# Kernel optimization log

Measured on AMD Instinct MI355X. Metric: run time of the kernel, lower is better.

## Reference

```python
import jax, jax.numpy as jnp
import numpy as np


def setup_inputs() -> dict:
    key = jax.random.key(0)
    ks = jax.random.split(key, 11)
    B, S, D, K = 8, 2048, 512, 256
    s = lambda k, shp, fan: jax.random.normal(k, shp, dtype=jnp.float32) / np.sqrt(fan)
    return {
        "x": jax.random.normal(ks[0], (B, S, D), dtype=jnp.float32),
        "Wk1": s(ks[1], (D, K), D), "bk1": jnp.zeros((K,), jnp.float32),
        "Wq1": s(ks[2], (D, K), D), "bq1": jnp.zeros((K,), jnp.float32),
        "Wk2": s(ks[3], (D, K), D), "bk2": jnp.zeros((K,), jnp.float32),
        "Wq2": s(ks[4], (D, K), D), "bq2": jnp.zeros((K,), jnp.float32),
        "Wv2": s(ks[5], (D, D), D), "bv2": jnp.zeros((D,), jnp.float32),
    }


def _attn(q, k, v):
    # raw scores with NO 1/sqrt(d) scaling, softmax over key axis, then AV
    scores = jax.nn.softmax(jnp.einsum('bqd,bkd->bqk', q, k), axis=-1)
    return jnp.einsum('bqk,bkd->bqd', scores, v)


def _block2(h, Wk2, bk2, Wq2, bq2, Wv2, bv2):
    k = h @ Wk2 + bk2
    q = h @ Wq2 + bq2
    v = h @ Wv2 + bv2
    v = v / jnp.linalg.norm(v, axis=2, keepdims=True)  # L2-normalize values
    return _attn(q, k, v)


def reference(x, Wk1, bk1, Wq1, bq1, Wk2, bk2, Wq2, bq2, Wv2, bv2):
    # block 1: values are the raw input x
    k1 = x @ Wk1 + bk1
    q1 = x @ Wq1 + bq1
    outputs = _attn(q1, k1, x)
    # blocks 2 and 3 reuse the SAME layer-2 weights (as in the torch forward)
    hidden = _block2(outputs, Wk2, bk2, Wq2, bq2, Wv2, bv2)
    final = _block2(hidden, Wk2, bk2, Wq2, bq2, Wv2, bv2)
    return final[0, -1, :]
```

## Files before the change

kernel.cpp:

```cpp
#include <hip/hip_runtime.h>
#include <math.h>

typedef __attribute__((ext_vector_type(8))) short short8;
typedef __attribute__((ext_vector_type(4))) float f32x4;
typedef unsigned short ushort_t;

__device__ inline unsigned short f2bf_rn(float f) {
    unsigned u = __builtin_bit_cast(unsigned, f);
    u += 0x7FFF + ((u >> 16) & 1);
    return (unsigned short)(u >> 16);
}
__device__ inline float bf2f(unsigned short h) {
    unsigned u = ((unsigned)h) << 16;
    return __builtin_bit_cast(float, u);
}

#define ISSUE(ST, RA, RB)                                                      \
  do {                                                                         \
    int s_ = (ST);                                                             \
    int sg_ = s_ / SPS;                                                        \
    int k0_ = (s_ - sg_ * SPS) * 64;                                           \
    const unsigned short* Ap_ = (sg_ < 2) ? Ah : Al;                           \
    const unsigned short* Bp_ = (sg_ == 1) ? Bl : Bh;                          \
    _Pragma("unroll") for (int i_ = 0; i_ < 4; ++i_) {                         \
      RA[i_] = *(const uint4*)(Ap_ + (size_t)(bm + crow[i_]) * lda + k0_ + csl[i_] * 8); \
      RB[i_] = *(const uint4*)(Bp_ + (size_t)(bn + crow[i_]) * ldb + k0_ + csl[i_] * 8); \
    }                                                                          \
  } while (0)

#define PHASE(IT, RWa, RWb, RLa, RLb)                                          \
  do {                                                                         \
    _Pragma("unroll") for (int i_ = 0; i_ < 4; ++i_) {                         \
      int wsl_ = csl[i_] ^ (crow[i_] & 7);                                     \
      *(uint4*)&As[crow[i_]][wsl_ * 8] = RWa[i_];                              \
      *(uint4*)&Bs[crow[i_]][wsl_ * 8] = RWb[i_];                              \
    }                                                                          \
    if ((IT) + 1 < CHUNK) { ISSUE(st0 + (IT) + 1, RLa, RLb); }                 \
    asm volatile("s_waitcnt lgkmcnt(0)\n\ts_barrier" ::: "memory");            \
    _Pragma("unroll") for (int kk = 0; kk < 2; ++kk) {                         \
      short8 af[4], bf[4];                                                     \
      _Pragma("unroll") for (int f = 0; f < 4; ++f) {                          \
        int ar = wm * 64 + f * 16 + r15;                                       \
        int as_ = (kk * 4 + ksl) ^ (ar & 7);                                   \
        af[f] = *(const short8*)&As[ar][as_ * 8];                              \
        int br = wn * 64 + f * 16 + r15;                                       \
        int bs_ = (kk * 4 + ksl) ^ (br & 7);                                   \
        bf[f] = *(const short8*)&Bs[br][bs_ * 8];                              \
      }                                                                        \
      _Pragma("unroll") for (int i_ = 0; i_ < 4; ++i_)                         \
        _Pragma("unroll") for (int j_ = 0; j_ < 4; ++j_)                       \
          acc[i_][j_] = __builtin_amdgcn_mfma_f32_16x16x32_bf16(               \
              af[i_], bf[j_], acc[i_][j_], 0, 0, 0);                           \
    }                                                                          \
    asm volatile("s_barrier" ::: "memory");                                    \
  } while (0)

template <int KSEG, int NSPLIT>
__global__ __launch_bounds__(256, 2) void gemm_bf16(
    const unsigned short* __restrict__ Ah, const unsigned short* __restrict__ Al, int lda,
    const unsigned short* __restrict__ Bh, const unsigned short* __restrict__ Bl, int ldb,
    float* __restrict__ Cout, int ldc)
{
    constexpr int SPS = KSEG / 64;
    constexpr int NST = 3 * SPS;
    constexpr int CHUNK = NST / NSPLIT;

    __shared__ __align__(16) unsigned short As[128][64];
    __shared__ __align__(16) unsigned short Bs[128][64];

    const int tid = threadIdx.x, lane = tid & 63, w = tid >> 6;
    const int wm = w >> 1, wn = w & 1;
    const int bm = blockIdx.y * 128, bn = blockIdx.x * 128;
    const int st0 = blockIdx.z * CHUNK;
    const int r15 = lane & 15, ksl = lane >> 4;

    int crow[4], csl[4];
#pragma unroll
    for (int i = 0; i < 4; ++i) { int c = tid + i * 256; crow[i] = c >> 3; csl[i] = c & 7; }

    f32x4 acc[4][4];
#pragma unroll
    for (int i = 0; i < 4; ++i)
#pragma unroll
        for (int j = 0; j < 4; ++j) acc[i][j] = (f32x4){0.f, 0.f, 0.f, 0.f};

    uint4 rA0[4], rB0[4], rA1[4], rB1[4];
    ISSUE(st0, rA0, rB0);

#pragma unroll 1
    for (int it = 0; it < CHUNK; it += 2) {
        PHASE(it,     rA0, rB0, rA1, rB1);
        PHASE(it + 1, rA1, rB1, rA0, rB0);
    }

    float* Cz = Cout + (size_t)blockIdx.z * (size_t)(gridDim.y * 128) * ldc;
#pragma unroll
    for (int i = 0; i < 4; ++i) {
        int rowb = bm + wm * 64 + i * 16 + (lane >> 4) * 4;
#pragma unroll
        for (int j = 0; j < 4; ++j) {
            int colb = bn + wn * 64 + j * 16 + r15;
#pragma unroll
            for (int r = 0; r < 4; ++r)
                Cz[(size_t)(rowb + r) * ldc + colb] = acc[i][j][r];
        }
    }
}

template <int NS, bool BIAS>
__global__ __launch_bounds__(256) void reduce_kernel(
    const float* __restrict__ part, size_t pstride4,
    const float* __restrict__ bias, float* __restrict__ C,
    unsigned short* __restrict__ Ch, unsigned short* __restrict__ Cl, int N)
{
    size_t idx = (size_t)blockIdx.x * 256 + threadIdx.x;
    const float4* p = (const float4*)part;
    float4 s = p[idx];
#pragma unroll
    for (int z = 1; z < NS; ++z) {
        float4 t = p[idx + (size_t)z * pstride4];
        s.x += t.x; s.y += t.y; s.z += t.z; s.w += t.w;
    }
    if (BIAS) {
        int col = (int)((idx * 4) & (size_t)(N - 1));
        s.x += bias[col]; s.y += bias[col + 1]; s.z += bias[col + 2]; s.w += bias[col + 3];
    }
    ((float4*)C)[idx] = s;
    float v[4] = {s.x, s.y, s.z, s.w};
    unsigned short h[4], l[4];
#pragma unroll
    for (int q = 0; q < 4; ++q) { h[q] = f2bf_rn(v[q]); l[q] = f2bf_rn(v[q] - bf2f(h[q])); }
    uint2 hp = make_uint2((unsigned)h[0] | ((unsigned)h[1] << 16), (unsigned)h[2] | ((unsigned)h[3] << 16));
    uint2 lp = make_uint2((unsigned)l[0] | ((unsigned)l[1] << 16), (unsigned)l[2] | ((unsigned)l[3] << 16));
    ((uint2*)Ch)[idx] = hp;
    ((uint2*)Cl)[idx] = lp;
}

#define SLK(r, s) ((s) ^ (((s) >> 3) & 3) ^ ((((r) ^ ((r) >> 3))) & 7))

__global__ __launch_bounds__(256, 2) void flash_attn(
    const unsigned short* __restrict__ Qh, const unsigned short* __restrict__ Ql,
    const unsigned short* __restrict__ Kh, const unsigned short* __restrict__ Kl,
    int ldqk,
    const unsigned short* __restrict__ VTh, const unsigned short* __restrict__ VTl,
    float* __restrict__ Opart, float* __restrict__ Mpart, float* __restrict__ Lpart)
{
    const int tid = threadIdx.x, lane = tid & 63, w = tid >> 6;
    const int z = blockIdx.x;
    const int q0 = blockIdx.y * 64;
    const int s0 = z * 256;
    const int cc = lane & 15, g = lane >> 4;

    __shared__ __align__(16) unsigned short KsH[32][256], KsL[32][256];
    __shared__ __align__(16) unsigned short PsH[64][32], PsL[64][32];
    __shared__ float Fs[64];
    __shared__ int flagAny[4];

    short8 qh[8], qlv[8];
#pragma unroll
    for (int ks = 0; ks < 8; ++ks) {
        const size_t qoff = (size_t)(q0 + w * 16 + cc) * ldqk + ks * 32 + g * 8;
        qh[ks]  = *(const short8*)(Qh + qoff);
        qlv[ks] = *(const short8*)(Ql + qoff);
    }

    f32x4 acc[4][8];
#pragma unroll
    for (int a = 0; a < 4; ++a)
#pragma unroll
        for (int b = 0; b < 8; ++b) acc[a][b] = (f32x4){0.f, 0.f, 0.f, 0.f};
    float m[4] = {-1e30f, -1e30f, -1e30f, -1e30f};
    float l[4] = {0.f, 0.f, 0.f, 0.f};

#pragma unroll 1
    for (int sub = 0; sub < 8; ++sub) {
        __syncthreads();
#pragma unroll
        for (int i = 0; i < 4; ++i) {
            int idx = tid + i * 256;
            int row = (idx >> 3) & 31;
            int sl  = (idx & 7) | ((idx >> 8) << 3);
            size_t go = (size_t)(s0 + sub * 32 + row) * ldqk + sl * 8;
            uint4 vh = *(const uint4*)(Kh + go);
            uint4 vl = *(const uint4*)(Kl + go);
            int sw = SLK(row, sl);
            *(uint4*)&KsH[row][sw * 8] = vh;
            *(uint4*)&KsL[row][sw * 8] = vl;
        }
        __syncthreads();

        f32x4 sac[2];
        sac[0] = (f32x4){0.f, 0.f, 0.f, 0.f};
        sac[1] = (f32x4){0.f, 0.f, 0.f, 0.f};
#pragma unroll
        for (int ks = 0; ks < 8; ++ks) {
#pragma unroll
            for (int t = 0; t < 2; ++t) {
                int row = t * 16 + cc;
                int sw = SLK(row, ks * 4 + g);
                short8 bh = *(const short8*)&KsH[row][sw * 8];
                short8 bl = *(const short8*)&KsL[row][sw * 8];
                sac[t] = __builtin_amdgcn_mfma_f32_16x16x32_bf16(qh[ks], bh, sac[t], 0, 0, 0);
                sac[t] = __builtin_amdgcn_mfma_f32_16x16x32_bf16(qh[ks], bl, sac[t], 0, 0, 0);
                sac[t] = __builtin_amdgcn_mfma_f32_16x16x32_bf16(qlv[ks], bh, sac[t], 0, 0, 0);
            }
        }

        float mt[4], fr[4];
        bool nb = false;
#pragma unroll
        for (int r = 0; r < 4; ++r) {
            float v = fmaxf(sac[0][r], sac[1][r]);
#pragma unroll
            for (int o = 8; o >= 1; o >>= 1) v = fmaxf(v, __shfl_xor(v, o));
            mt[r] = v;
            nb = nb || (v > m[r] + 8.f);
        }
        const int need = __any((int)nb);
        if (need) {
#pragma unroll
            for (int r = 0; r < 4; ++r) {
                float mn = fmaxf(m[r], mt[r]);
                fr[r] = __expf(m[r] - mn);
                m[r] = mn;
                l[r] *= fr[r];
            }
        } else {
#pragma unroll
            for (int r = 0; r < 4; ++r) fr[r] = 1.f;
        }
        if (cc == 0) {
#pragma unroll
            for (int r = 0; r < 4; ++r) Fs[w * 16 + g * 4 + r] = fr[r];
        }
        if (lane == 0) flagAny[w] = need;

#pragma unroll
        for (int t = 0; t < 2; ++t) {
            float ps[4];
#pragma unroll
            for (int r = 0; r < 4; ++r) {
                float p = __expf(sac[t][r] - m[r]);
                ps[r] = p;
                unsigned short ph = f2bf_rn(p);
                unsigned short pl = f2bf_rn(p - bf2f(ph));
                int qq = w * 16 + g * 4 + r;
                int kv = cc + 16 * t;
                int col = (((kv >> 3) ^ (qq & 3)) << 3) | (kv & 7);
                PsH[qq][col] = ph;
                PsL[qq][col] = pl;
            }
#pragma unroll
            for (int r = 0; r < 4; ++r) {
                float s = ps[r];
#pragma unroll
                for (int o = 8; o >= 1; o >>= 1) s += __shfl_xor(s, o);
                l[r] += s;
            }
        }
        __syncthreads();

        int anyf = flagAny[0] | flagAny[1] | flagAny[2] | flagAny[3];
        if (anyf) {
#pragma unroll
            for (int qt = 0; qt < 4; ++qt)
#pragma unroll
                for (int r = 0; r < 4; ++r) {
                    float fq = Fs[qt * 16 + g * 4 + r];
#pragma unroll
                    for (int dt = 0; dt < 8; ++dt) acc[qt][dt][r] *= fq;
                }
        }

        short8 pah[4], pal[4];
#pragma unroll
        for (int qt = 0; qt < 4; ++qt) {
            int qr = qt * 16 + cc;
            int col = (g ^ (qr & 3)) << 3;
            pah[qt] = *(const short8*)&PsH[qr][col];
            pal[qt] = *(const short8*)&PsL[qr][col];
        }
#pragma unroll
        for (int dt = 0; dt < 8; ++dt) {
            size_t vo = (size_t)(w * 128 + dt * 16 + cc) * 2048 + s0 + sub * 32 + g * 8;
            short8 vh = *(const short8*)(VTh + vo);
            short8 vl = *(const short8*)(VTl + vo);
#pragma unroll
            for (int qt = 0; qt < 4; ++qt) {
                acc[qt][dt] = __builtin_amdgcn_mfma_f32_16x16x32_bf16(pah[qt], vh, acc[qt][dt], 0, 0, 0);
                acc[qt][dt] = __builtin_amdgcn_mfma_f32_16x16x32_bf16(pah[qt], vl, acc[qt][dt], 0, 0, 0);
                acc[qt][dt] = __builtin_amdgcn_mfma_f32_16x16x32_bf16(pal[qt], vh, acc[qt][dt], 0, 0, 0);
            }
        }
    }

#pragma unroll
    for (int qt = 0; qt < 4; ++qt)
#pragma unroll
        for (int dt = 0; dt < 8; ++dt)
#pragma unroll
            for (int r = 0; r < 4; ++r) {
                int row = q0 + qt * 16 + g * 4 + r;
                int col = w * 128 + dt * 16 + cc;
                Opart[((size_t)z * 2048 + row) * 512 + col] = acc[qt][dt][r];
            }
    if (cc == 0) {
#pragma unroll
        for (int r = 0; r < 4; ++r) {
            int row = q0 + w * 16 + g * 4 + r;
            Mpart[z * 2048 + row] = m[r];
            Lpart[z * 2048 + row] = l[r];
        }
    }
}

__global__ __launch_bounds__(256) void flash_combine(
    const float* __restrict__ Opart, const float* __restrict__ Mpart,
    const float* __restrict__ Lpart,
    unsigned short* __restrict__ Oh, unsigned short* __restrict__ Ol)
{
    const int q = blockIdx.x;
    const int tid = threadIdx.x;
    float wz[8];
    float mstar = -1e30f;
#pragma unroll
    for (int zz = 0; zz < 8; ++zz) { wz[zz] = Mpart[zz * 2048 + q]; mstar = fmaxf(mstar, wz[zz]); }
    float L = 0.f;
#pragma unroll
    for (int zz = 0; zz < 8; ++zz) {
        float e = __expf(wz[zz] - mstar);
        L += e * Lpart[zz * 2048 + q];
        wz[zz] = e;
    }
    float invL = 1.f / L;
    int d = tid * 2;
    float sx = 0.f, sy = 0.f;
#pragma unroll
    for (int zz = 0; zz < 8; ++zz) {
        const float2 t = *(const float2*)(Opart + ((size_t)zz * 2048 + q) * 512 + d);
        sx += wz[zz] * t.x;
        sy += wz[zz] * t.y;
    }
    sx *= invL; sy *= invL;
    unsigned short h0 = f2bf_rn(sx), h1 = f2bf_rn(sy);
    unsigned short l0 = f2bf_rn(sx - bf2f(h0)), l1 = f2bf_rn(sy - bf2f(h1));
    *(unsigned*)(Oh + (size_t)q * 512 + d) = (unsigned)h0 | ((unsigned)h1 << 16);
    *(unsigned*)(Ol + (size_t)q * 512 + d) = (unsigned)l0 | ((unsigned)l1 << 16);
}

__global__ __launch_bounds__(256) void l2norm_kernel(float* __restrict__ V, int ld,
                                                     int coloff, int D)
{
    __shared__ float red[8];
    const int tid = threadIdx.x;
    float* p = V + (size_t)blockIdx.x * ld + coloff;
    float s = 0.f;
    for (int i = tid; i < D; i += 256) { float v = p[i]; s = fmaf(v, v, s); }
#pragma unroll
    for (int o = 32; o; o >>= 1) s += __shfl_down(s, o);
    if ((tid & 63) == 0) red[tid >> 6] = s;
    __syncthreads();
    float scale = 1.f / sqrtf(red[0] + red[1] + red[2] + red[3]);
    for (int i = tid; i < D; i += 256) p[i] *= scale;
}

__global__ __launch_bounds__(256) void tc_kernel(
    const float* __restrict__ in, int ldin,
    unsigned short* __restrict__ oh, unsigned short* __restrict__ ol,
    int ldo, int rowoff)
{
    __shared__ float tile[32][33];
    int bx = blockIdx.x * 32, by = blockIdx.y * 32;
    int tx = threadIdx.x & 31, ty = threadIdx.x >> 5;
#pragma unroll
    for (int i = 0; i < 32; i += 8)
        tile[ty + i][tx] = in[(size_t)(by + ty + i) * ldin + bx + tx];
    __syncthreads();
#pragma unroll
    for (int i = 0; i < 32; i += 8) {
        float v = tile[tx][ty + i];
        unsigned short h = f2bf_rn(v);
        unsigned short l = f2bf_rn(v - bf2f(h));
        size_t o = (size_t)(rowoff + bx + ty + i) * ldo + by + tx;
        oh[o] = h; ol[o] = l;
    }
}

__global__ __launch_bounds__(256) void convert_hl(
    const float* __restrict__ in, unsigned short* __restrict__ oh,
    unsigned short* __restrict__ ol)
{
    size_t idx = (size_t)blockIdx.x * 256 + threadIdx.x;
    float4 s = ((const float4*)in)[idx];
    float v[4] = {s.x, s.y, s.z, s.w};
    unsigned short h[4], l[4];
#pragma unroll
    for (int q = 0; q < 4; ++q) { h[q] = f2bf_rn(v[q]); l[q] = f2bf_rn(v[q] - bf2f(h[q])); }
    uint2 hp = make_uint2((unsigned)h[0] | ((unsigned)h[1] << 16), (unsigned)h[2] | ((unsigned)h[3] << 16));
    uint2 lp = make_uint2((unsigned)l[0] | ((unsigned)l[1] << 16), (unsigned)l[2] | ((unsigned)l[3] << 16));
    ((uint2*)oh)[idx] = hp;
    ((uint2*)ol)[idx] = lp;
}

__global__ __launch_bounds__(256) void concat_bias(
    const float* bk1, const float* bq1, const float* bk2, const float* bq2,
    const float* bv2, float* b1, float* b2)
{
    int i = blockIdx.x * 256 + threadIdx.x;
    if (i < 512) b1[i] = (i < 256) ? bk1[i] : bq1[i - 256];
    if (i < 1024) b2[i] = (i < 256) ? bk2[i] : (i < 512 ? bq2[i - 256] : bv2[i - 512]);
}

template <bool HAS_BIAS>
__global__ __launch_bounds__(256) void gemv_nt(
    const float* __restrict__ a, const float* __restrict__ Bt, int ldb,
    const float* __restrict__ bias, float* __restrict__ out, int K)
{
    int w = threadIdx.x >> 6, lane = threadIdx.x & 63;
    int n = blockIdx.x * 4 + w;
    const float* row = Bt + (size_t)n * ldb;
    float s = 0.f;
    for (int k = lane; k < K; k += 64) s = fmaf(a[k], row[k], s);
#pragma unroll
    for (int o = 32; o; o >>= 1) s += __shfl_down(s, o);
    if (lane == 0) out[n] = HAS_BIAS ? s + bias[n] : s;
}

__global__ __launch_bounds__(256) void gemv_hl(
    const float* __restrict__ p, const unsigned short* __restrict__ Vh,
    const unsigned short* __restrict__ Vl, int ld, float* __restrict__ out, int K)
{
    int w = threadIdx.x >> 6, lane = threadIdx.x & 63;
    int d = blockIdx.x * 4 + w;
    const unsigned short* rh = Vh + (size_t)d * ld;
    const unsigned short* rl = Vl + (size_t)d * ld;
    float s = 0.f;
    for (int k = lane; k < K; k += 64) s = fmaf(p[k], bf2f(rh[k]) + bf2f(rl[k]), s);
#pragma unroll
    for (int o = 32; o; o >>= 1) s += __shfl_down(s, o);
    if (lane == 0) out[d] = s;
}

__global__ __launch_bounds__(256) void softmax_f32(float* __restrict__ S, int L)
{
    __shared__ float row[2048];
    __shared__ float red[8];
    const int tid = threadIdx.x;
    float* p = S + (size_t)blockIdx.x * L;
    float mx = -1e30f;
    for (int i = tid; i < L; i += 256) { float v = p[i]; row[i] = v; mx = fmaxf(mx, v); }
#pragma unroll
    for (int o = 32; o; o >>= 1) mx = fmaxf(mx, __shfl_down(mx, o));
    if ((tid & 63) == 0) red[tid >> 6] = mx;
    __syncthreads();
    mx = fmaxf(fmaxf(red[0], red[1]), fmaxf(red[2], red[3]));
    float sum = 0.f;
    for (int i = tid; i < L; i += 256) { float e = expf(row[i] - mx); row[i] = e; sum += e; }
#pragma unroll
    for (int o = 32; o; o >>= 1) sum += __shfl_down(sum, o);
    __syncthreads();
    if ((tid & 63) == 0) red[4 + (tid >> 6)] = sum;
    __syncthreads();
    float inv = 1.f / (red[4] + red[5] + red[6] + red[7]);
    for (int i = tid; i < L; i += 256) p[i] = row[i] * inv;
}

extern "C" void kernel_launch(void* const* d_in, const int* in_sizes, int n_in,
                              void* d_out, int out_size, void* d_ws, size_t ws_size,
                              hipStream_t stream)
{
    const float* x   = (const float*)d_in[0];
    const float* Wk1 = (const float*)d_in[1];
    const float* bk1 = (const float*)d_in[2];
    const float* Wq1 = (const float*)d_in[3];
    const float* bq1 = (const float*)d_in[4];
    const float* Wk2 = (const float*)d_in[5];
    const float* bk2 = (const float*)d_in[6];
    const float* Wq2 = (const float*)d_in[7];
    const float* bq2 = (const float*)d_in[8];
    const float* Wv2 = (const float*)d_in[9];
    const float* bv2 = (const float*)d_in[10];
    float* out = (float*)d_out;

    const int S = 2048, D = 512;
    typedef unsigned short us;

    char* p = (char*)d_ws;
    float* C   = (float*)p;  p += (size_t)S * 1024 * 4;
    float* BIG = (float*)p;  p += (size_t)8 * S * 512 * 4;
    float* Mp  = (float*)p;  p += (size_t)8 * S * 4;
    float* Lp  = (float*)p;  p += (size_t)8 * S * 4;
    us* Chh = (us*)p; p += (size_t)S * 1024 * 2;
    us* Cll = (us*)p; p += (size_t)S * 1024 * 2;
    us* Hh  = (us*)p; p += (size_t)S * D * 2;
    us* Hl  = (us*)p; p += (size_t)S * D * 2;
    us* xh  = (us*)p; p += (size_t)S * D * 2;
    us* xl  = (us*)p; p += (size_t)S * D * 2;
    us* VTh = (us*)p; p += (size_t)D * S * 2;
    us* VTl = (us*)p; p += (size_t)D * S * 2;
    us* WT1h = (us*)p; p += (size_t)512 * 512 * 2;
    us* WT1l = (us*)p; p += (size_t)512 * 512 * 2;
    us* WT2h = (us*)p; p += (size_t)1024 * 512 * 2;
    us* WT2l = (us*)p; p += (size_t)1024 * 512 * 2;
    float* b1 = (float*)p; p += 512 * 4;
    float* b2 = (float*)p; p += 1024 * 4;

    dim3 blk(256);
    const size_t PSTR  = (size_t)S * 512 / 4;
    const size_t PSTR2 = (size_t)S * 1024 / 4;

    convert_hl<<<dim3(S * D / 1024), blk, 0, stream>>>(x, xh, xl);
    tc_kernel<<<dim3(16, 64), blk, 0, stream>>>(x, 512, VTh, VTl, S, 0);
    tc_kernel<<<dim3(8, 16), blk, 0, stream>>>(Wk1, 256, WT1h, WT1l, 512, 0);
    tc_kernel<<<dim3(8, 16), blk, 0, stream>>>(Wq1, 256, WT1h, WT1l, 512, 256);
    tc_kernel<<<dim3(8, 16), blk, 0, stream>>>(Wk2, 256, WT2h, WT2l, 512, 0);
    tc_kernel<<<dim3(8, 16), blk, 0, stream>>>(Wq2, 256, WT2h, WT2l, 512, 256);
    tc_kernel<<<dim3(16, 16), blk, 0, stream>>>(Wv2, 512, WT2h, WT2l, 512, 512);
    concat_bias<<<dim3(4), blk, 0, stream>>>(bk1, bq1, bk2, bq2, bv2, b1, b2);

    gemm_bf16<512, 3><<<dim3(4, 16, 3), blk, 0, stream>>>(xh, xl, 512, WT1h, WT1l, 512, BIG, 512);
    reduce_kernel<3, true><<<dim3(S * 512 / 1024), blk, 0, stream>>>(BIG, PSTR, b1, C, Chh, Cll, 512);
    flash_attn<<<dim3(8, 32), blk, 0, stream>>>(Chh + 256, Cll + 256, Chh, Cll, 512,
                                                VTh, VTl, BIG, Mp, Lp);
    flash_combine<<<dim3(S), blk, 0, stream>>>(BIG, Mp, Lp, Hh, Hl);

    gemm_bf16<512, 2><<<dim3(8, 16, 2), blk, 0, stream>>>(Hh, Hl, 512, WT2h, WT2l, 512, BIG, 1024);
    reduce_kernel<2, true><<<dim3(S * 1024 / 1024), blk, 0, stream>>>(BIG, PSTR2, b2, C, Chh, Cll, 1024);
    l2norm_kernel<<<dim3(S), blk, 0, stream>>>(C, 1024, 512, 512);
    tc_kernel<<<dim3(16, 64), blk, 0, stream>>>(C + 512, 1024, VTh, VTl, S, 0);
    flash_attn<<<dim3(8, 32), blk, 0, stream>>>(Chh + 256, Cll + 256, Chh, Cll, 1024,
                                                VTh, VTl, BIG, Mp, Lp);
    flash_combine<<<dim3(S), blk, 0, stream>>>(BIG, Mp, Lp, Hh, Hl);

    gemm_bf16<512, 2><<<dim3(8, 16, 2), blk, 0, stream>>>(Hh, Hl, 512, WT2h, WT2l, 512, BIG, 1024);
    reduce_kernel<2, true><<<dim3(S * 1024 / 1024), blk, 0, stream>>>(BIG, PSTR2, b2, C, Chh, Cll, 1024);
    l2norm_kernel<<<dim3(S), blk, 0, stream>>>(C, 1024, 512, 512);
    tc_kernel<<<dim3(16, 64), blk, 0, stream>>>(C + 512, 1024, VTh, VTl, S, 0);
    gemv_nt<false><<<dim3(S / 4), blk, 0, stream>>>(C + (size_t)(S - 1) * 1024 + 256, C, 1024,
                                                    nullptr, BIG, 256);
    softmax_f32<<<dim3(1), blk, 0, stream>>>(BIG, S);
    gemv_hl<<<dim3(D / 4), blk, 0, stream>>>(BIG, VTh, VTl, S, out, S);
}
```

Measured before the change: 482.3 us.

## Split flash attention over value dims, raise split-K, fuse L2 norm into reduce

The flash attention grid gains a z dimension that splits the 512 value columns into two halves. This doubles the block count and halves the per-thread accumulator registers, at the cost of recomputing QK scores and softmax in both halves. The split-K factor of the projection GEMMs is raised (3→6, 2→4) to expose more parallelism, which adds partial-sum traffic in the reduce step. The separate l2norm kernel is removed and its row normalization of the value columns is folded into the reduce kernel via a block reduction, saving one launch and one pass over C.

```diff
diff --git a/kernel.cpp b/kernel.cpp
--- a/kernel.cpp
+++ b/kernel.cpp
@@ -3,7 +3,7 @@
 
 typedef __attribute__((ext_vector_type(8))) short short8;
 typedef __attribute__((ext_vector_type(4))) float f32x4;
-typedef unsigned short ushort_t;
+typedef unsigned short us;
 
 __device__ inline unsigned short f2bf_rn(float f) {
     unsigned u = __builtin_bit_cast(unsigned, f);
@@ -107,13 +107,15 @@
     }
 }
 
-template <int NS, bool BIAS>
+template <int NS, bool BIAS, bool L2N>
 __global__ __launch_bounds__(256) void reduce_kernel(
     const float* __restrict__ part, size_t pstride4,
     const float* __restrict__ bias, float* __restrict__ C,
     unsigned short* __restrict__ Ch, unsigned short* __restrict__ Cl, int N)
 {
-    size_t idx = (size_t)blockIdx.x * 256 + threadIdx.x;
+    __shared__ float red[4];
+    const int tid = threadIdx.x;
+    size_t idx = (size_t)blockIdx.x * 256 + tid;
     const float4* p = (const float4*)part;
     float4 s = p[idx];
 #pragma unroll
@@ -124,6 +126,17 @@
     if (BIAS) {
         int col = (int)((idx * 4) & (size_t)(N - 1));
         s.x += bias[col]; s.y += bias[col + 1]; s.z += bias[col + 2]; s.w += bias[col + 3];
+    }
+    if (L2N) {
+        float ss = (tid >= 128) ? (s.x * s.x + s.y * s.y + s.z * s.z + s.w * s.w) : 0.f;
+#pragma unroll
+        for (int o = 32; o; o >>= 1) ss += __shfl_down(ss, o);
+        if ((tid & 63) == 0) red[tid >> 6] = ss;
+        __syncthreads();
+        if (tid >= 128) {
+            float scale = 1.f / sqrtf(red[2] + red[3]);
+            s.x *= scale; s.y *= scale; s.z *= scale; s.w *= scale;
+        }
     }
     ((float4*)C)[idx] = s;
     float v[4] = {s.x, s.y, s.z, s.w};
@@ -148,8 +161,10 @@
     const int tid = threadIdx.x, lane = tid & 63, w = tid >> 6;
     const int z = blockIdx.x;
     const int q0 = blockIdx.y * 64;
+    const int dblk = blockIdx.z;
     const int s0 = z * 256;
     const int cc = lane & 15, g = lane >> 4;
+    const int dbase = dblk * 256 + w * 64;
 
     __shared__ __align__(16) unsigned short KsH[32][256], KsL[32][256];
     __shared__ __align__(16) unsigned short PsH[64][32], PsL[64][32];
@@ -164,11 +179,11 @@
         qlv[ks] = *(const short8*)(Ql + qoff);
     }
 
-    f32x4 acc[4][8];
+    f32x4 acc[4][4];
 #pragma unroll
     for (int a = 0; a < 4; ++a)
 #pragma unroll
-        for (int b = 0; b < 8; ++b) acc[a][b] = (f32x4){0.f, 0.f, 0.f, 0.f};
+        for (int b = 0; b < 4; ++b) acc[a][b] = (f32x4){0.f, 0.f, 0.f, 0.f};
     float m[4] = {-1e30f, -1e30f, -1e30f, -1e30f};
     float l[4] = {0.f, 0.f, 0.f, 0.f};
 
@@ -240,10 +255,10 @@
             float ps[4];
 #pragma unroll
             for (int r = 0; r < 4; ++r) {
-                float p = __expf(sac[t][r] - m[r]);
-                ps[r] = p;
-                unsigned short ph = f2bf_rn(p);
-                unsigned short pl = f2bf_rn(p - bf2f(ph));
+                float pv = __expf(sac[t][r] - m[r]);
+                ps[r] = pv;
+                unsigned short ph = f2bf_rn(pv);
+                unsigned short pl = f2bf_rn(pv - bf2f(ph));
                 int qq = w * 16 + g * 4 + r;
                 int kv = cc + 16 * t;
                 int col = (((kv >> 3) ^ (qq & 3)) << 3) | (kv & 7);
@@ -252,10 +267,10 @@
             }
 #pragma unroll
             for (int r = 0; r < 4; ++r) {
-                float s = ps[r];
-#pragma unroll
-                for (int o = 8; o >= 1; o >>= 1) s += __shfl_xor(s, o);
-                l[r] += s;
+                float sv = ps[r];
+#pragma unroll
+                for (int o = 8; o >= 1; o >>= 1) sv += __shfl_xor(sv, o);
+                l[r] += sv;
             }
         }
         __syncthreads();
@@ -268,7 +283,7 @@
                 for (int r = 0; r < 4; ++r) {
                     float fq = Fs[qt * 16 + g * 4 + r];
 #pragma unroll
-                    for (int dt = 0; dt < 8; ++dt) acc[qt][dt][r] *= fq;
+                    for (int dt = 0; dt < 4; ++dt) acc[qt][dt][r] *= fq;
                 }
         }
 
@@ -281,8 +296,8 @@
             pal[qt] = *(const short8*)&PsL[qr][col];
         }
 #pragma unroll
-        for (int dt = 0; dt < 8; ++dt) {
-            size_t vo = (size_t)(w * 128 + dt * 16 + cc) * 2048 + s0 + sub * 32 + g * 8;
+        for (int dt = 0; dt < 4; ++dt) {
+            size_t vo = (size_t)(dbase + dt * 16 + cc) * 2048 + s0 + sub * 32 + g * 8;
             short8 vh = *(const short8*)(VTh + vo);
             short8 vl = *(const short8*)(VTl + vo);
 #pragma unroll
@@ -297,14 +312,14 @@
 #pragma unroll
     for (int qt = 0; qt < 4; ++qt)
 #pragma unroll
-        for (int dt = 0; dt < 8; ++dt)
+        for (int dt = 0; dt < 4; ++dt)
 #pragma unroll
             for (int r = 0; r < 4; ++r) {
                 int row = q0 + qt * 16 + g * 4 + r;
-                int col = w * 128 + dt * 16 + cc;
+                int col = dbase + dt * 16 + cc;
                 Opart[((size_t)z * 2048 + row) * 512 + col] = acc[qt][dt][r];
             }
-    if (cc == 0) {
+    if (dblk == 0 && cc == 0) {
 #pragma unroll
         for (int r = 0; r < 4; ++r) {
             int row = q0 + w * 16 + g * 4 + r;
@@ -346,22 +361,6 @@
     unsigned short l0 = f2bf_rn(sx - bf2f(h0)), l1 = f2bf_rn(sy - bf2f(h1));
     *(unsigned*)(Oh + (size_t)q * 512 + d) = (unsigned)h0 | ((unsigned)h1 << 16);
     *(unsigned*)(Ol + (size_t)q * 512 + d) = (unsigned)l0 | ((unsigned)l1 << 16);
-}
-
-__global__ __launch_bounds__(256) void l2norm_kernel(float* __restrict__ V, int ld,
-                                                     int coloff, int D)
-{
-    __shared__ float red[8];
-    const int tid = threadIdx.x;
-    float* p = V + (size_t)blockIdx.x * ld + coloff;
-    float s = 0.f;
-    for (int i = tid; i < D; i += 256) { float v = p[i]; s = fmaf(v, v, s); }
-#pragma unroll
-    for (int o = 32; o; o >>= 1) s += __shfl_down(s, o);
-    if ((tid & 63) == 0) red[tid >> 6] = s;
-    __syncthreads();
-    float scale = 1.f / sqrtf(red[0] + red[1] + red[2] + red[3]);
-    for (int i = tid; i < D; i += 256) p[i] *= scale;
 }
 
 __global__ __launch_bounds__(256) void tc_kernel(
@@ -483,7 +482,6 @@
     float* out = (float*)d_out;
 
     const int S = 2048, D = 512;
-    typedef unsigned short us;
 
     char* p = (char*)d_ws;
     float* C   = (float*)p;  p += (size_t)S * 1024 * 4;
@@ -518,23 +516,21 @@
     tc_kernel<<<dim3(16, 16), blk, 0, stream>>>(Wv2, 512, WT2h, WT2l, 512, 512);
     concat_bias<<<dim3(4), blk, 0, stream>>>(bk1, bq1, bk2, bq2, bv2, b1, b2);
 
-    gemm_bf16<512, 3><<<dim3(4, 16, 3), blk, 0, stream>>>(xh, xl, 512, WT1h, WT1l, 512, BIG, 512);
-    reduce_kernel<3, true><<<dim3(S * 512 / 1024), blk, 0, stream>>>(BIG, PSTR, b1, C, Chh, Cll, 512);
-    flash_attn<<<dim3(8, 32), blk, 0, stream>>>(Chh + 256, Cll + 256, Chh, Cll, 512,
-                                                VTh, VTl, BIG, Mp, Lp);
+    gemm_bf16<512, 6><<<dim3(4, 16, 6), blk, 0, stream>>>(xh, xl, 512, WT1h, WT1l, 512, BIG, 512);
+    reduce_kernel<6, true, false><<<dim3(S * 512 / 1024), blk, 0, stream>>>(BIG, PSTR, b1, C, Chh, Cll, 512);
+    flash_attn<<<dim3(8, 32, 2), blk, 0, stream>>>(Chh + 256, Cll + 256, Chh, Cll, 512,
+                                                   VTh, VTl, BIG, Mp, Lp);
     flash_combine<<<dim3(S), blk, 0, stream>>>(BIG, Mp, Lp, Hh, Hl);
 
-    gemm_bf16<512, 2><<<dim3(8, 16, 2), blk, 0, stream>>>(Hh, Hl, 512, WT2h, WT2l, 512, BIG, 1024);
-    reduce_kernel<2, true><<<dim3(S * 1024 / 1024), blk, 0, stream>>>(BIG, PSTR2, b2, C, Chh, Cll, 1024);
-    l2norm_kernel<<<dim3(S), blk, 0, stream>>>(C, 1024, 512, 512);
+    gemm_bf16<512, 4><<<dim3(8, 16, 4), blk, 0, stream>>>(Hh, Hl, 512, WT2h, WT2l, 512, BIG, 1024);
+    reduce_kernel<4, true, true><<<dim3(S * 1024 / 1024), blk, 0, stream>>>(BIG, PSTR2, b2, C, Chh, Cll, 1024);
     tc_kernel<<<dim3(16, 64), blk, 0, stream>>>(C + 512, 1024, VTh, VTl, S, 0);
-    flash_attn<<<dim3(8, 32), blk, 0, stream>>>(Chh + 256, Cll + 256, Chh, Cll, 1024,
-                                                VTh, VTl, BIG, Mp, Lp);
+    flash_attn<<<dim3(8, 32, 2), blk, 0, stream>>>(Chh + 256, Cll + 256, Chh, Cll, 1024,
+                                                   VTh, VTl, BIG, Mp, Lp);
     flash_combine<<<dim3(S), blk, 0, stream>>>(BIG, Mp, Lp, Hh, Hl);
 
-    gemm_bf16<512, 2><<<dim3(8, 16, 2), blk, 0, stream>>>(Hh, Hl, 512, WT2h, WT2l, 512, BIG, 1024);
-    reduce_kernel<2, true><<<dim3(S * 1024 / 1024), blk, 0, stream>>>(BIG, PSTR2, b2, C, Chh, Cll, 1024);
-    l2norm_kernel<<<dim3(S), blk, 0, stream>>>(C, 1024, 512, 512);
+    gemm_bf16<512, 4><<<dim3(8, 16, 4), blk, 0, stream>>>(Hh, Hl, 512, WT2h, WT2l, 512, BIG, 1024);
+    reduce_kernel<4, true, true><<<dim3(S * 1024 / 1024), blk, 0, stream>>>(BIG, PSTR2, b2, C, Chh, Cll, 1024);
     tc_kernel<<<dim3(16, 64), blk, 0, stream>>>(C + 512, 1024, VTh, VTl, S, 0);
     gemv_nt<false><<<dim3(S / 4), blk, 0, stream>>>(C + (size_t)(S - 1) * 1024 + 256, C, 1024,
                                                     nullptr, BIG, 256);
```

Measured after the change: 389.5 us. -19.2%, faster.
